# Kernel optimization log

Measured on AMD Instinct MI355X. Metric: run time of the kernel, lower is better.

The kernel has to match this reference:

```python
import jax, jax.numpy as jnp
import numpy as np
import math

H, C = 16, 4


def _clustering(x, alv, mu, log_var, log_prior, mi_estimation):
    # x: [B,h,L,D], alv: [B,h,L], mu/log_var: [h or 1, C, D], log_prior: [h or 1, C]
    B, Hh, L, D = x.shape
    z = x  # eval mode: no reparameterization noise
    zd = z[:, :, :, None, :]                       # [B,h,L,1,D]
    mu_b = mu[:, None, :, :]                       # [h,1,C,D]
    lv = log_var[:, None, :, :]
    var = jnp.exp(lv)
    lp = jax.nn.log_softmax(log_prior, axis=-1)    # [h,C]
    mse = (zd - mu_b) ** 2 / var                   # [B,h,L,C,D]
    log_pdf = -0.5 * mse.sum(-1) - 0.5 * lv.sum(-1) - D * math.pi  # [B,h,L,C]
    log_pdf = log_pdf + lp[:, None, :]
    shift = jax.lax.stop_gradient(log_pdf.max(axis=-1, keepdims=True))
    log_probs = jax.nn.log_softmax(log_pdf - shift + 5.0, axis=-1)
    cp = jnp.exp(log_probs)                        # cluster probs [B,h,L,C]
    lp_b = jnp.broadcast_to(lp[None, :, None, :], log_probs.shape)
    # F.kl_div(log_probs, prior) = prior * (log prior - log_probs)
    kl = (jnp.exp(lp_b) * (lp_b - log_probs)).sum(-1).mean(axis=(1, 2))
    alv5 = alv[:, :, :, None, None]
    avar = jnp.exp(alv5)
    kl = kl + 0.5 * (cp * (mse + avar / var + lv).sum(-1)).sum(-1).mean(axis=(1, 2))
    kl = kl - 0.5 * ((1.0 + alv5).sum(-1) * D).mean(axis=(1, 2, 3))
    eye = jnp.eye(L, dtype=x.dtype)
    div = jnp.einsum('bhqc,bhkc->bhqk', cp, cp)
    div = ((div - eye) ** 2) * (eye * 1.25 + (1.0 - eye) * 0.75)
    div_loss = div.mean(axis=(1, 2, 3))
    if mi_estimation:
        pdf = jnp.exp(log_pdf - jax.lax.stop_gradient(log_pdf.max())).sum(-1, keepdims=True)
        w = cp * pdf
        mi_probs = w / jnp.maximum(w.sum(axis=2, keepdims=True), 1e-6)  # L1 normalize over L
        mi_p = jnp.minimum(jnp.einsum('bilc,bjlc->blij', mi_probs, cp), 1.0)
        mask_h = 1.0 - jnp.eye(Hh, dtype=x.dtype)
        mi_loss = -(jnp.log(1.0 - mi_p + 1e-6) * mask_h).mean(axis=(1, 2, 3)) * 10.0
        aff = jnp.einsum('bhqc,bhkc->bhqk', cp, cp)
        diag = jnp.diagonal(jax.nn.log_softmax(aff, axis=-1), axis1=2, axis2=3)
        mi_loss = mi_loss - diag.mean(axis=(1, 2))
    else:
        mi_loss = jnp.zeros_like(kl)
    return z, cp, kl, div_loss, mi_loss


def _forward(query, key, value, Wq, bq, Wk, bk, Wv, bv, Wo, bo, Wsem, bsem,
             Whead, bhead, tok_mu, tok_log_var, tok_log_prior,
             head_mu, head_log_var, head_log_prior):
    B, L, D = query.shape
    Dk = D // H
    q = query @ Wq + bq
    k = key @ Wk + bk
    v = value @ Wv + bv
    alv = (q @ Wsem + bsem).transpose(0, 2, 1)                 # [B,H,L]
    qh = q.reshape(B, L, H, Dk).transpose(0, 2, 1, 3)          # [B,H,L,Dk]
    z, cp_q, kl_q, div_q, _ = _clustering(qh, alv, tok_mu, tok_log_var, tok_log_prior, False)
    kh = k.reshape(B, L, H, Dk).transpose(0, 2, 1, 3)
    vh = v.reshape(B, L, H, Dk).transpose(0, 2, 1, 3)
    cluster_mask = jnp.einsum('bhqc,bhkc->bhqk', cp_q, cp_q)   # token-cluster affinity mask
    scores = jnp.einsum('bhqd,bhkd->bhqk', z, kh) / math.sqrt(Dk)
    attn = jax.nn.softmax(scores, axis=-1) * cluster_mask
    attn = attn / (attn.sum(axis=-1, keepdims=True) + 1e-6)
    ctx = jnp.einsum('bhqk,bhkd->bhqd', attn, vh)              # [B,H,L,Dk]
    ctx_f = ctx.transpose(0, 2, 1, 3).reshape(B, L, D)
    alv_h = (ctx_f @ Whead + bhead).transpose(0, 2, 1)         # [B,H,L]
    _, cp_h, kl_h, div_h, mi = _clustering(ctx, alv_h, head_mu, head_log_var, head_log_prior, True)
    out = ctx_f @ Wo + bo
    return out, attn.mean(axis=1), kl_q + kl_h, div_q + div_h, mi


def setup_inputs() -> dict:
    key = jax.random.key(0)
    ks = jax.random.split(key, 12)
    B, L, D = 8, 512, 1024
    Dk = D // H
    s = 1.0 / math.sqrt(D)
    f32 = jnp.float32
    inp = {
        'query': jax.random.normal(ks[0], (B, L, D), f32),
        'key': jax.random.normal(ks[1], (B, L, D), f32),
        'value': jax.random.normal(ks[2], (B, L, D), f32),
        'Wq': jax.random.normal(ks[3], (D, D), f32) * s, 'bq': jnp.zeros((D,), f32),
        'Wk': jax.random.normal(ks[4], (D, D), f32) * s, 'bk': jnp.zeros((D,), f32),
        'Wv': jax.random.normal(ks[5], (D, D), f32) * s, 'bv': jnp.zeros((D,), f32),
        'Wo': jax.random.normal(ks[6], (D, D), f32) * s, 'bo': jnp.zeros((D,), f32),
        'Wsem': jax.random.normal(ks[7], (D, H), f32) * s, 'bsem': jnp.zeros((H,), f32),
        'Whead': jax.random.normal(ks[8], (D, H), f32) * s, 'bhead': jnp.zeros((H,), f32),
        'tok_mu': jax.random.normal(ks[9], (H, C, Dk), f32) * 0.1,
        'tok_log_var': jnp.zeros((H, C, Dk), f32),
        'tok_log_prior': jnp.full((H, C), math.log(1.0 / C), f32),
        'head_mu': jax.random.normal(ks[10], (1, C, Dk), f32) * 0.1,
        'head_log_var': jnp.zeros((1, C, Dk), f32),
        'head_log_prior': jnp.full((1, C), math.log(1.0 / C), f32),
    }
    return inp


def reference(query, key, value, Wq, bq, Wk, bk, Wv, bv, Wo, bo, Wsem, bsem,
              Whead, bhead, tok_mu, tok_log_var, tok_log_prior,
              head_mu, head_log_var, head_log_prior):
    return _forward(query, key, value, Wq, bq, Wk, bk, Wv, bv, Wo, bo, Wsem, bsem,
                    Whead, bhead, tok_mu, tok_log_var, tok_log_prior,
                    head_mu, head_log_var, head_log_prior)
```

## Files before the change

kernel.cpp:

```cpp
#include <hip/hip_runtime.h>
#include <math.h>

#define BB 8
#define LL 512
#define DD 1024
#define HH 16
#define CC 4
#define DK 64
#define NEG_DPI 201.06192982974676f

typedef __attribute__((ext_vector_type(8))) short short8;
typedef __attribute__((ext_vector_type(4))) float floatx4;
typedef __attribute__((ext_vector_type(8))) unsigned short u16x8;
typedef __attribute__((ext_vector_type(4))) unsigned short u16x4;

__device__ inline float block_sum256(float v, float* s_red) {
    int t = threadIdx.x;
    s_red[t] = v; __syncthreads();
    for (int off = 128; off > 0; off >>= 1) {
        if (t < off) s_red[t] += s_red[t + off];
        __syncthreads();
    }
    float r = s_red[0]; __syncthreads();
    return r;
}
__device__ inline float block_max256(float v, float* s_red) {
    int t = threadIdx.x;
    s_red[t] = v; __syncthreads();
    for (int off = 128; off > 0; off >>= 1) {
        if (t < off) s_red[t] = fmaxf(s_red[t], s_red[t + off]);
        __syncthreads();
    }
    float r = s_red[0]; __syncthreads();
    return r;
}
__device__ inline unsigned int fenc(float f) {
    unsigned int b = __float_as_uint(f);
    return (b & 0x80000000u) ? ~b : (b | 0x80000000u);
}
__device__ inline float fdec(unsigned int u) {
    return (u & 0x80000000u) ? __uint_as_float(u ^ 0x80000000u) : __uint_as_float(~u);
}
__device__ inline unsigned short f2bf(float x) {
    unsigned int u = __float_as_uint(x);
    return (unsigned short)((u + 0x7FFFu + ((u >> 16) & 1u)) >> 16);
}
__device__ inline float bf2f(unsigned short h) {
    return __uint_as_float((unsigned int)h << 16);
}

__global__ __launch_bounds__(256)
void convert_hilo(const float* __restrict__ x, unsigned short* __restrict__ hh,
                  unsigned short* __restrict__ ll) {
    int i = blockIdx.x * 256 + threadIdx.x;
    float4 v = ((const float4*)x)[i];
    u16x4 h, l;
    float c[4] = {v.x, v.y, v.z, v.w};
#pragma unroll
    for (int j = 0; j < 4; j++) {
        unsigned short hb = f2bf(c[j]);
        h[j] = hb;
        l[j] = f2bf(c[j] - bf2f(hb));
    }
    ((u16x4*)hh)[i] = h;
    ((u16x4*)ll)[i] = l;
}

__global__ __launch_bounds__(256)
void wconv4(const float* __restrict__ W0, const float* __restrict__ W1,
            const float* __restrict__ W2, const float* __restrict__ W3,
            unsigned short* __restrict__ Tbase) {
    __shared__ float tile[64][65];
    int z = blockIdx.z;
    const float* W = (z == 0) ? W0 : (z == 1) ? W1 : (z == 2) ? W2 : W3;
    const size_t WS = (size_t)DD * DD;
    unsigned short* Th = Tbase + (size_t)z * 2 * WS;
    unsigned short* Tl = Th + WS;
    int t = threadIdx.x;
    int n0 = blockIdx.x * 64, k0 = blockIdx.y * 64;
    int r = t >> 4, c4 = (t & 15) * 4;
#pragma unroll
    for (int rr = 0; rr < 64; rr += 16) {
        float4 v = *(const float4*)&W[(size_t)(k0 + r + rr) * DD + n0 + c4];
        tile[r + rr][c4 + 0] = v.x; tile[r + rr][c4 + 1] = v.y;
        tile[r + rr][c4 + 2] = v.z; tile[r + rr][c4 + 3] = v.w;
    }
    __syncthreads();
    int rn = t >> 2, kg = (t & 3) * 16;
    u16x8 oh[2], ol[2];
#pragma unroll
    for (int j = 0; j < 16; j++) {
        float x = tile[kg + j][rn];
        unsigned short hb = f2bf(x);
        oh[j >> 3][j & 7] = hb;
        ol[j >> 3][j & 7] = f2bf(x - bf2f(hb));
    }
    size_t o = (size_t)(n0 + rn) * DD + k0 + kg;
    *(u16x8*)&Th[o] = oh[0]; *(u16x8*)&Th[o + 8] = oh[1];
    *(u16x8*)&Tl[o] = ol[0]; *(u16x8*)&Tl[o + 8] = ol[1];
}

__device__ __forceinline__
void gemm_body(const unsigned short* __restrict__ Ah, const unsigned short* __restrict__ Al,
               const unsigned short* __restrict__ Bh, const unsigned short* __restrict__ Bl,
               const float* __restrict__ bias, float* __restrict__ C,
               unsigned short* __restrict__ Ch, unsigned short* __restrict__ Cl) {
    __shared__ unsigned short sAh[128 * 32];
    __shared__ unsigned short sAl[128 * 32];
    __shared__ unsigned short sBh[128 * 32];
    __shared__ unsigned short sBl[128 * 32];
    int t = threadIdx.x;
    int n0 = blockIdx.x * 128, m0 = blockIdx.y * 128;
    int lane = t & 63, w = t >> 6;
    int wm = w >> 1, wn = w & 1;
    int lm = lane & 15, quad = lane >> 4;
    int srow = t >> 1, sk = (t & 1) * 16;

    const unsigned short* gAh = Ah + (size_t)(m0 + srow) * DD + sk;
    const unsigned short* gAl = Al + (size_t)(m0 + srow) * DD + sk;
    const unsigned short* gBh = Bh + (size_t)(n0 + srow) * DD + sk;
    const unsigned short* gBl = Bl + (size_t)(n0 + srow) * DD + sk;
    unsigned short* wAh = &sAh[srow * 32 + sk];
    unsigned short* wAl = &sAl[srow * 32 + sk];
    unsigned short* wBh = &sBh[srow * 32 + sk];
    unsigned short* wBl = &sBl[srow * 32 + sk];

    floatx4 acc[4][4] = {};

    for (int kt = 0; kt < 32; kt++) {
        int kb = kt * 32;
        u16x8 a0 = *(const u16x8*)(gAh + kb);
        u16x8 a1 = *(const u16x8*)(gAh + kb + 8);
        u16x8 a2 = *(const u16x8*)(gAl + kb);
        u16x8 a3 = *(const u16x8*)(gAl + kb + 8);
        u16x8 b0 = *(const u16x8*)(gBh + kb);
        u16x8 b1 = *(const u16x8*)(gBh + kb + 8);
        u16x8 b2 = *(const u16x8*)(gBl + kb);
        u16x8 b3 = *(const u16x8*)(gBl + kb + 8);
        __syncthreads();
        *(u16x8*)(wAh) = a0; *(u16x8*)(wAh + 8) = a1;
        *(u16x8*)(wAl) = a2; *(u16x8*)(wAl + 8) = a3;
        *(u16x8*)(wBh) = b0; *(u16x8*)(wBh + 8) = b1;
        *(u16x8*)(wBl) = b2; *(u16x8*)(wBl + 8) = b3;
        __syncthreads();

        short8 bh[4], bl[4];
#pragma unroll
        for (int j = 0; j < 4; j++) {
            int nb = (wn * 64 + j * 16 + lm) * 32 + quad * 8;
            bh[j] = *(const short8*)&sBh[nb];
            bl[j] = *(const short8*)&sBl[nb];
        }
#pragma unroll
        for (int i = 0; i < 4; i++) {
            int ab = (wm * 64 + i * 16 + lm) * 32 + quad * 8;
            short8 ah = *(const short8*)&sAh[ab];
            short8 al = *(const short8*)&sAl[ab];
#pragma unroll
            for (int j = 0; j < 4; j++) {
                acc[i][j] = __builtin_amdgcn_mfma_f32_16x16x32_bf16(ah, bh[j], acc[i][j], 0, 0, 0);
                acc[i][j] = __builtin_amdgcn_mfma_f32_16x16x32_bf16(ah, bl[j], acc[i][j], 0, 0, 0);
                acc[i][j] = __builtin_amdgcn_mfma_f32_16x16x32_bf16(al, bh[j], acc[i][j], 0, 0, 0);
            }
        }
    }
#pragma unroll
    for (int i = 0; i < 4; i++) {
#pragma unroll
        for (int j = 0; j < 4; j++) {
            int n = n0 + wn * 64 + j * 16 + lm;
            float bv = bias[n];
#pragma unroll
            for (int r = 0; r < 4; r++) {
                int m = m0 + wm * 64 + i * 16 + quad * 4 + r;
                size_t idx = (size_t)m * DD + n;
                float val = acc[i][j][r] + bv;
                if (C) C[idx] = val;
                if (Ch) {
                    unsigned short hb = f2bf(val);
                    Ch[idx] = hb;
                    Cl[idx] = f2bf(val - bf2f(hb));
                }
            }
        }
    }
}

__global__ __launch_bounds__(256)
void mfma_gemm_bias(const unsigned short* __restrict__ Ah, const unsigned short* __restrict__ Al,
                    const unsigned short* __restrict__ Bh, const unsigned short* __restrict__ Bl,
                    const float* __restrict__ bias, float* __restrict__ C,
                    unsigned short* __restrict__ Ch, unsigned short* __restrict__ Cl) {
    gemm_body(Ah, Al, Bh, Bl, bias, C, Ch, Cl);
}

__global__ __launch_bounds__(256)
void mfma_gemm_qkv(const unsigned short* __restrict__ ist3, const unsigned short* __restrict__ wbase,
                   const float* __restrict__ bq, const float* __restrict__ bk,
                   const float* __restrict__ bv, float* __restrict__ Cq,
                   unsigned short* __restrict__ obase) {
    int z = blockIdx.z;
    const size_t NB = (size_t)BB * LL * DD;
    const size_t WS = (size_t)DD * DD;
    const unsigned short* Ah = ist3 + (size_t)z * 2 * NB;
    const unsigned short* Bh = wbase + (size_t)z * 2 * WS;
    const float* bias = (z == 0) ? bq : (z == 1) ? bk : bv;
    float* C = (z == 0) ? Cq : nullptr;
    unsigned short* Ch = obase + (size_t)z * 2 * NB;
    gemm_body(Ah, Ah + NB, Bh, Bh + WS, bias, C, Ch, Ch + NB);
}

__global__ __launch_bounds__(256)
void vt_prep2(const unsigned short* __restrict__ voh, const unsigned short* __restrict__ vol,
              unsigned short* __restrict__ vth, unsigned short* __restrict__ vtl) {
    __shared__ unsigned short tile[128 * 68];
    int t = threadIdx.x;
    int which = blockIdx.x & 1;
    int l0 = (blockIdx.x >> 1) * 128, h = blockIdx.y, b = blockIdx.z;
    const unsigned short* src = which ? vol : voh;
    unsigned short* dst = which ? vtl : vth;
#pragma unroll
    for (int i = 0; i < 8; i++) {
        int u = t + i * 256;
        int l = u >> 4, c4 = (u & 15) * 4;
        u16x4 v4 = *(const u16x4*)&src[((size_t)(b * LL + l0 + l)) * DD + h * DK + c4];
        tile[l * 68 + c4 + 0] = v4[0]; tile[l * 68 + c4 + 1] = v4[1];
        tile[l * 68 + c4 + 2] = v4[2]; tile[l * 68 + c4 + 3] = v4[3];
    }
    __syncthreads();
    size_t ob = ((size_t)(b * HH + h)) * DK * LL;
#pragma unroll
    for (int i = 0; i < 8; i++) {
        int u = t + i * 256;
        int d = u >> 5, lq = (u & 31) * 4;
        u16x4 o;
#pragma unroll
        for (int j = 0; j < 4; j++) o[j] = tile[(lq + j) * 68 + d];
        *(u16x4*)&dst[ob + (size_t)d * LL + l0 + lq] = o;
    }
}

__global__ __launch_bounds__(256)
void alv_gemm(const float* __restrict__ A, const float* __restrict__ Wp,
              const float* __restrict__ bias, float* __restrict__ alv) {
    __shared__ float As[16][65];
    __shared__ float Ws[64][17];
    int t = threadIdx.x;
    int m0 = blockIdx.x * 16;
    int r = t >> 4, hh = t & 15;
    float acc = 0.f;
    for (int kt = 0; kt < 16; kt++) {
        __syncthreads();
#pragma unroll
        for (int i = 0; i < 4; i++) {
            int e = t + i * 256;
            int rr = e >> 6, kk = e & 63;
            As[rr][kk] = A[(size_t)(m0 + rr) * DD + kt * 64 + kk];
        }
#pragma unroll
        for (int i = 0; i < 4; i++) {
            int e = t + i * 256;
            int kk = e >> 4, h2 = e & 15;
            Ws[kk][h2] = Wp[(size_t)(kt * 64 + kk) * HH + h2];
        }
        __syncthreads();
#pragma unroll
        for (int kk = 0; kk < 64; kk++) acc += As[r][kk] * Ws[kk][hh];
    }
    int m = m0 + r;
    int b = m >> 9, l = m & 511;
    alv[(size_t)(b * HH + hh) * LL + l] = acc + bias[hh];
}

__global__ __launch_bounds__(256)
void cluster_kernel(const float* __restrict__ zsrc, const float* __restrict__ alv,
                    const float* __restrict__ mu, const float* __restrict__ logvar,
                    const float* __restrict__ logprior,
                    float* __restrict__ cp_out, float* __restrict__ lpdf_out,
                    unsigned int* __restrict__ maxenc, float* __restrict__ kl_out,
                    int isHead) {
    __shared__ float s_mu[CC * DK], s_iv[CC * DK], s_lv[CC * DK];
    __shared__ float s_slv[CC], s_siv[CC], s_lp[CC];
    __shared__ float s_red[256];
    int t = threadIdx.x;
    int tile = blockIdx.x & 1;
    int bh = blockIdx.x >> 1;
    int h = bh & (HH - 1), b = bh >> 4;
    int hm = isHead ? 0 : h;

    {
        float m = mu[hm * CC * DK + t];
        float lv = logvar[hm * CC * DK + t];
        s_mu[t] = m; s_lv[t] = lv; s_iv[t] = expf(-lv);
    }
    __syncthreads();
    if (t < CC) {
        float slv = 0.f, siv = 0.f;
        for (int d = 0; d < DK; d++) { slv += s_lv[t * DK + d]; siv += s_iv[t * DK + d]; }
        s_slv[t] = slv; s_siv[t] = siv;
    }
    if (t == CC) {
        float x[CC];
        float m = -1e30f;
        for (int c = 0; c < CC; c++) { x[c] = logprior[hm * CC + c]; m = fmaxf(m, x[c]); }
        float se = 0.f;
        for (int c = 0; c < CC; c++) se += expf(x[c] - m);
        float lse = m + logf(se);
        for (int c = 0; c < CC; c++) s_lp[c] = x[c] - lse;
    }
    __syncthreads();

    int l = tile * 256 + t;
    const float* zp = zsrc + ((size_t)(b * LL + l)) * DD + h * DK;
    float acc[CC] = {0.f, 0.f, 0.f, 0.f};
    for (int d = 0; d < DK; d += 4) {
        float4 z4 = *(const float4*)(zp + d);
#pragma unroll
        for (int c = 0; c < CC; c++) {
            float d0 = z4.x - s_mu[c * DK + d];     acc[c] += d0 * d0 * s_iv[c * DK + d];
            float d1 = z4.y - s_mu[c * DK + d + 1]; acc[c] += d1 * d1 * s_iv[c * DK + d + 1];
            float d2 = z4.z - s_mu[c * DK + d + 2]; acc[c] += d2 * d2 * s_iv[c * DK + d + 2];
            float d3 = z4.w - s_mu[c * DK + d + 3]; acc[c] += d3 * d3 * s_iv[c * DK + d + 3];
        }
    }
    float lpdf[CC];
#pragma unroll
    for (int c = 0; c < CC; c++)
        lpdf[c] = -0.5f * acc[c] - 0.5f * s_slv[c] - NEG_DPI + s_lp[c];
    float m = fmaxf(fmaxf(lpdf[0], lpdf[1]), fmaxf(lpdf[2], lpdf[3]));
    float se = 0.f;
#pragma unroll
    for (int c = 0; c < CC; c++) se += expf(lpdf[c] - m);
    float lse = m + logf(se);
    float lprob[CC], cpv[CC];
    size_t idx = ((size_t)(bh * LL + l)) * CC;
#pragma unroll
    for (int c = 0; c < CC; c++) {
        lprob[c] = lpdf[c] - lse;
        cpv[c] = expf(lprob[c]);
        cp_out[idx + c] = cpv[c];
    }
    if (isHead) {
#pragma unroll
        for (int c = 0; c < CC; c++) lpdf_out[idx + c] = lpdf[c];
    }
    float alvv = alv[(size_t)bh * LL + l];
    float avar = expf(alvv);
    float t1 = 0.f, t2 = 0.f;
#pragma unroll
    for (int c = 0; c < CC; c++) {
        t1 += expf(s_lp[c]) * (s_lp[c] - lprob[c]);
        t2 += cpv[c] * (acc[c] + avar * s_siv[c] + s_slv[c]);
    }
    float klv = t1 + 0.5f * t2 - 0.5f * (float)DK * (1.0f + alvv);
    float tot = block_sum256(klv, s_red);
    if (t == 0) atomicAdd(kl_out + b, tot * (1.0f / (HH * LL)));
    if (isHead) {
        float mt = block_max256(m, s_red);
        if (t == 0) atomicMax(maxenc, fenc(mt));
    }
}

__global__ __launch_bounds__(256)
void pairstats_kernel(const float* __restrict__ cp, float* __restrict__ div_out,
                      float* __restrict__ mi_out, int isHead) {
    __shared__ float s_cp[LL * CC];
    __shared__ float s_red[256];
    int t = threadIdx.x;
    int bh = blockIdx.x >> 3;
    int seg = blockIdx.x & 7;
    int b = bh >> 4;
    const float* base = cp + (size_t)bh * LL * CC;
#pragma unroll
    for (int i = 0; i < 2; i++) {
        int e = t + i * 256;
        *(float4*)&s_cp[e * 4] = *(const float4*)&base[e * 4];
    }
    __syncthreads();

    int q = seg * 64 + (t >> 2);
    int ln = t & 3;
    float4 cq = *(float4*)&s_cp[q * 4];
    float divacc = 0.f, m = -1e30f, s = 0.f, selfdot = 0.f;
    for (int k = ln; k < LL; k += 4) {
        float4 ck = *(float4*)&s_cp[k * 4];
        float dot = cq.x * ck.x + cq.y * ck.y + cq.z * ck.z + cq.w * ck.w;
        float del = (k == q) ? 1.f : 0.f;
        float dd = dot - del;
        divacc += dd * dd * (0.75f + 0.5f * del);
        if (isHead) {
            if (dot > m) { s = s * expf(m - dot) + 1.f; m = dot; }
            else         { s += expf(dot - m); }
            if (k == q) selfdot = dot;
        }
    }
#pragma unroll
    for (int off = 1; off <= 2; off <<= 1) divacc += __shfl_xor(divacc, off, 64);
    float diag = 0.f;
    if (isHead) {
#pragma unroll
        for (int off = 1; off <= 2; off <<= 1) {
            float om = __shfl_xor(m, off, 64);
            float os = __shfl_xor(s, off, 64);
            float nm = fmaxf(m, om);
            s = s * expf(m - nm) + os * expf(om - nm);
            m = nm;
        }
#pragma unroll
        for (int off = 1; off <= 2; off <<= 1) selfdot += __shfl_xor(selfdot, off, 64);
        diag = selfdot - (m + logf(s));
    }
    float dtot = block_sum256(ln == 0 ? divacc : 0.f, s_red);
    if (t == 0) atomicAdd(div_out + b, dtot * (1.0f / ((float)HH * LL * LL)));
    if (isHead) {
        float gtot = block_sum256(ln == 0 ? diag : 0.f, s_red);
        if (t == 0) atomicAdd(mi_out + b, -gtot * (1.0f / (HH * LL)));
    }
}

__global__ __launch_bounds__(256)
void attn3_kernel(const unsigned short* __restrict__ qoh, const unsigned short* __restrict__ qol,
                  const unsigned short* __restrict__ koh, const unsigned short* __restrict__ kol,
                  const unsigned short* __restrict__ vth, const unsigned short* __restrict__ vtl,
                  const float* __restrict__ cpq,
                  float* __restrict__ ctxf, unsigned short* __restrict__ cxh,
                  unsigned short* __restrict__ cxl,
                  float* __restrict__ attn_h, int h0) {
    __shared__ __align__(16) char sbuf[33280];
    __shared__ float s_inv[16];
    float* S = (float*)sbuf;
    unsigned short* Ph = (unsigned short*)sbuf;
    unsigned short* Pl = Ph + 16 * 520;

    int t = threadIdx.x;
    int id = blockIdx.x;
    int xcd = id & 7;
    int sid = id >> 3;
    int qt = sid & 31;
    int combo = ((sid >> 5) << 3) | xcd;
    int hl = combo & 7;
    int b = combo >> 3;
    int h = h0 + hl;
    int q0 = qt * 16;
    int lane = t & 63, w = t >> 6;
    int lm = lane & 15, quad = lane >> 4;
    int bh = b * HH + h;

    size_t qbase = ((size_t)(b * LL + q0 + lm)) * DD + h * DK + quad * 8;
    short8 qah0 = *(const short8*)(qoh + qbase);
    short8 qah1 = *(const short8*)(qoh + qbase + 32);
    short8 qal0 = *(const short8*)(qol + qbase);
    short8 qal1 = *(const short8*)(qol + qbase + 32);

    floatx4 sa[8] = {};
#pragma unroll
    for (int j = 0; j < 8; j++) {
        int n0 = w * 128 + j * 16;
        size_t kbase = ((size_t)(b * LL + n0 + lm)) * DD + h * DK + quad * 8;
        short8 kbh0 = *(const short8*)(koh + kbase);
        short8 kbh1 = *(const short8*)(koh + kbase + 32);
        short8 kbl0 = *(const short8*)(kol + kbase);
        short8 kbl1 = *(const short8*)(kol + kbase + 32);
        sa[j] = __builtin_amdgcn_mfma_f32_16x16x32_bf16(qah0, kbh0, sa[j], 0, 0, 0);
        sa[j] = __builtin_amdgcn_mfma_f32_16x16x32_bf16(qah1, kbh1, sa[j], 0, 0, 0);
        sa[j] = __builtin_amdgcn_mfma_f32_16x16x32_bf16(qah0, kbl0, sa[j], 0, 0, 0);
        sa[j] = __builtin_amdgcn_mfma_f32_16x16x32_bf16(qah1, kbl1, sa[j], 0, 0, 0);
        sa[j] = __builtin_amdgcn_mfma_f32_16x16x32_bf16(qal0, kbh0, sa[j], 0, 0, 0);
        sa[j] = __builtin_amdgcn_mfma_f32_16x16x32_bf16(qal1, kbh1, sa[j], 0, 0, 0);
    }
#pragma unroll
    for (int j = 0; j < 8; j++) {
        int kc = w * 128 + j * 16 + lm;
#pragma unroll
        for (int r = 0; r < 4; r++)
            S[(quad * 4 + r) * 516 + kc] = sa[j][r] * 0.125f;
    }
    __syncthreads();

    {
        int r = t >> 4, ln = t & 15;
        const float4* cpb = (const float4*)(cpq + (size_t)bh * LL * CC);
        float m = -1e30f;
        for (int k = ln; k < LL; k += 16) m = fmaxf(m, S[r * 516 + k]);
#pragma unroll
        for (int off = 8; off > 0; off >>= 1) m = fmaxf(m, __shfl_xor(m, off, 16));
        float4 cq = cpb[q0 + r];
        float Z = 0.f, Sm = 0.f;
        for (int k = ln; k < LL; k += 16) {
            float e = expf(S[r * 516 + k] - m);
            float4 ck = cpb[k];
            float mask = cq.x * ck.x + cq.y * ck.y + cq.z * ck.z + cq.w * ck.w;
            float a = e * mask;
            Z += e; Sm += a;
            S[r * 516 + k] = a;
        }
#pragma unroll
        for (int off = 8; off > 0; off >>= 1) {
            Z += __shfl_xor(Z, off, 16);
            Sm += __shfl_xor(Sm, off, 16);
        }
        if (ln == 0) s_inv[r] = 1.f / (Sm + 1e-6f * Z);
    }
    __syncthreads();

    float4 pv[8];
#pragma unroll
    for (int i = 0; i < 8; i++) {
        int e = t + i * 256;
        int r2 = e >> 7, k4 = (e & 127) * 4;
        float4 p = *(float4*)&S[r2 * 516 + k4];
        float inv = s_inv[r2];
        p.x *= inv; p.y *= inv; p.z *= inv; p.w *= inv;
        pv[i] = p;
        *(float4*)&attn_h[(((size_t)((b * 8 + hl) * LL + q0 + r2)) * LL) + k4] = p;
    }
    __syncthreads();
#pragma unroll
    for (int i = 0; i < 8; i++) {
        int e = t + i * 256;
        int r2 = e >> 7, k4 = (e & 127) * 4;
        float c[4] = {pv[i].x, pv[i].y, pv[i].z, pv[i].w};
        u16x4 hv, lv;
#pragma unroll
        for (int j = 0; j < 4; j++) {
            unsigned short hb = f2bf(c[j]);
            hv[j] = hb;
            lv[j] = f2bf(c[j] - bf2f(hb));
        }
        *(u16x4*)&Ph[r2 * 520 + k4] = hv;
        *(u16x4*)&Pl[r2 * 520 + k4] = lv;
    }
    __syncthreads();

    int dn = w * 16 + lm;
    const unsigned short* vrh = vth + ((size_t)bh * DK + dn) * LL;
    const unsigned short* vrl = vtl + ((size_t)bh * DK + dn) * LL;
    floatx4 ca = {};
#pragma unroll
    for (int kc = 0; kc < 16; kc++) {
        int kb = kc * 32 + quad * 8;
        short8 pah = *(const short8*)&Ph[lm * 520 + kb];
        short8 pal = *(const short8*)&Pl[lm * 520 + kb];
        short8 vbh = *(const short8*)(vrh + kb);
        short8 vbl = *(const short8*)(vrl + kb);
        ca = __builtin_amdgcn_mfma_f32_16x16x32_bf16(pah, vbh, ca, 0, 0, 0);
        ca = __builtin_amdgcn_mfma_f32_16x16x32_bf16(pah, vbl, ca, 0, 0, 0);
        ca = __builtin_amdgcn_mfma_f32_16x16x32_bf16(pal, vbh, ca, 0, 0, 0);
    }
#pragma unroll
    for (int r = 0; r < 4; r++) {
        float val = ca[r];
        size_t idx = ((size_t)(b * LL + q0 + quad * 4 + r)) * DD + h * DK + dn;
        ctxf[idx] = val;
        unsigned short hb = f2bf(val);
        cxh[idx] = hb;
        cxl[idx] = f2bf(val - bf2f(hb));
    }
}

__global__ __launch_bounds__(256)
void attn_reduce(const float* __restrict__ attn_h, float* __restrict__ attn_out,
                 int accumulate) {
    int e = blockIdx.x * 256 + threadIdx.x;
    int b = e >> 16;
    int rem = e & 65535;
    float4 s = {0.f, 0.f, 0.f, 0.f};
#pragma unroll
    for (int hl = 0; hl < 8; hl++) {
        float4 v = ((const float4*)attn_h)[(((size_t)(b * 8 + hl)) << 16) + rem];
        s.x += v.x; s.y += v.y; s.z += v.z; s.w += v.w;
    }
    float4* o = (float4*)attn_out + (((size_t)b) << 16) + rem;
    const float sc = 1.0f / (float)HH;
    float4 prev = {0.f, 0.f, 0.f, 0.f};
    if (accumulate) prev = *o;
    prev.x += s.x * sc; prev.y += s.y * sc; prev.z += s.z * sc; prev.w += s.w * sc;
    *o = prev;
}

__global__ __launch_bounds__(256)
void wsum_kernel(const float* __restrict__ lpdf, const float* __restrict__ cp,
                 const unsigned int* __restrict__ maxenc,
                 float* __restrict__ pdf_out, float* __restrict__ wsum_out) {
    __shared__ float s_red[256];
    int t = threadIdx.x;
    int bh = blockIdx.x;
    float M = fdec(*maxenc);
    float a[CC] = {0.f, 0.f, 0.f, 0.f};
    for (int li = 0; li < 2; li++) {
        int l = t + li * 256;
        size_t idx = ((size_t)bh * LL + l) * CC;
        float p0 = expf(lpdf[idx + 0] - M);
        float p1 = expf(lpdf[idx + 1] - M);
        float p2 = expf(lpdf[idx + 2] - M);
        float p3 = expf(lpdf[idx + 3] - M);
        float pd = p0 + p1 + p2 + p3;
        pdf_out[(size_t)bh * LL + l] = pd;
        a[0] += cp[idx + 0] * pd; a[1] += cp[idx + 1] * pd;
        a[2] += cp[idx + 2] * pd; a[3] += cp[idx + 3] * pd;
    }
#pragma unroll
    for (int c = 0; c < CC; c++) {
        float tot = block_sum256(a[c], s_red);
        if (t == 0) wsum_out[bh * CC + c] = tot;
    }
}

__global__ __launch_bounds__(256)
void mi_kernel(const float* __restrict__ cp, const float* __restrict__ pdf,
               const float* __restrict__ wsum, float* __restrict__ mi_out) {
    __shared__ float s_q[HH * CC];
    __shared__ float s_c[HH * CC];
    __shared__ float s_red[256];
    int t = threadIdx.x;
    int b = blockIdx.x >> 9;
    int l = blockIdx.x & 511;
    if (t < HH * CC) {
        int i = t >> 2, c = t & 3;
        float cpv = cp[((size_t)(b * HH + i) * LL + l) * CC + c];
        s_c[t] = cpv;
        float w = cpv * pdf[(size_t)(b * HH + i) * LL + l];
        float ws = wsum[(b * HH + i) * CC + c];
        s_q[t] = w / fmaxf(ws, 1e-6f);
    }
    __syncthreads();
    int i = t >> 4, j = t & 15;
    float sdot = 0.f;
#pragma unroll
    for (int c = 0; c < CC; c++) sdot += s_q[i * 4 + c] * s_c[j * 4 + c];
    float mi_p = fminf(sdot, 1.f);
    float val = (i != j) ? logf(1.f - mi_p + 1e-6f) : 0.f;
    float tot = block_sum256(val, s_red);
    if (t == 0) atomicAdd(mi_out + b, -10.f * tot * (1.0f / ((float)LL * HH * HH)));
}

extern "C" void kernel_launch(void* const* d_in, const int* in_sizes, int n_in,
                              void* d_out, int out_size, void* d_ws, size_t ws_size,
                              hipStream_t stream) {
    (void)in_sizes; (void)n_in; (void)out_size; (void)ws_size;
    const float* query  = (const float*)d_in[0];
    const float* key    = (const float*)d_in[1];
    const float* value  = (const float*)d_in[2];
    const float* Wq     = (const float*)d_in[3];
    const float* bq     = (const float*)d_in[4];
    const float* Wk     = (const float*)d_in[5];
    const float* bk     = (const float*)d_in[6];
    const float* Wv     = (const float*)d_in[7];
    const float* bv     = (const float*)d_in[8];
    const float* Wo     = (const float*)d_in[9];
    const float* bo     = (const float*)d_in[10];
    const float* Wsem   = (const float*)d_in[11];
    const float* bsem   = (const float*)d_in[12];
    const float* Whead  = (const float*)d_in[13];
    const float* bhead  = (const float*)d_in[14];
    const float* tokmu  = (const float*)d_in[15];
    const float* toklv  = (const float*)d_in[16];
    const float* toklp  = (const float*)d_in[17];
    const float* headmu = (const float*)d_in[18];
    const float* headlv = (const float*)d_in[19];
    const float* headlp = (const float*)d_in[20];

    float* ws   = (float*)d_ws;
    const size_t NBLD = (size_t)BB * LL * DD;
    float* q    = ws;
    float* ctxf = ws + NBLD;
    float* alvq = ws + 2 * NBLD;
    float* alvh = alvq + (size_t)BB * HH * LL;
    float* cpq  = alvh + (size_t)BB * HH * LL;
    float* cph  = cpq + (size_t)BB * HH * LL * CC;
    float* lpdfh= cph + (size_t)BB * HH * LL * CC;
    float* pdfb = lpdfh + (size_t)BB * HH * LL * CC;
    float* wsumb= pdfb + (size_t)BB * HH * LL;
    unsigned int* maxenc = (unsigned int*)(wsumb + (size_t)BB * HH * CC);
    float* scr3 = (float*)(maxenc + 4);

    unsigned short* us = (unsigned short*)(scr3 + (size_t)BB * 8 * LL * LL);
    const size_t WSZ = (size_t)DD * DD;
    unsigned short* ist_h = us;
    unsigned short* ist_l = ist_h + NBLD;
    unsigned short* qoh = ist_l + NBLD;
    unsigned short* qol = qoh + NBLD;
    unsigned short* koh = qol + NBLD;
    unsigned short* kol = koh + NBLD;
    unsigned short* voh = kol + NBLD;
    unsigned short* vol = voh + NBLD;
    unsigned short* vth = vol + NBLD;
    unsigned short* vtl = vth + NBLD;
    unsigned short* wqh = vtl + NBLD;
    unsigned short* wql = wqh + WSZ;
    unsigned short* wkh = wql + WSZ;
    unsigned short* wkl = wkh + WSZ;
    unsigned short* wvh = wkl + WSZ;
    unsigned short* wvl = wvh + WSZ;
    unsigned short* woh = wvl + WSZ;
    unsigned short* wol = woh + WSZ;

    unsigned short* ist3 = (unsigned short*)scr3;
    float* attn_h = scr3;

    float* out      = (float*)d_out;
    float* attn_out = out + NBLD;
    float* kl_out   = attn_out + (size_t)BB * LL * LL;
    float* div_out  = kl_out + BB;
    float* mi_out   = div_out + BB;

    hipMemsetAsync(kl_out, 0, 3 * BB * sizeof(float), stream);
    hipMemsetAsync(maxenc, 0, sizeof(unsigned int), stream);

    wconv4<<<dim3(16, 16, 4), 256, 0, stream>>>(Wq, Wk, Wv, Wo, wqh);

    convert_hilo<<<NBLD / 1024, 256, 0, stream>>>(query, ist3,            ist3 + NBLD);
    convert_hilo<<<NBLD / 1024, 256, 0, stream>>>(key,   ist3 + 2 * NBLD, ist3 + 3 * NBLD);
    convert_hilo<<<NBLD / 1024, 256, 0, stream>>>(value, ist3 + 4 * NBLD, ist3 + 5 * NBLD);
    mfma_gemm_qkv<<<dim3(DD / 128, BB * LL / 128, 3), 256, 0, stream>>>(
        ist3, wqh, bq, bk, bv, q, qoh);

    vt_prep2<<<dim3(2 * LL / 128, HH, BB), 256, 0, stream>>>(voh, vol, vth, vtl);

    alv_gemm<<<BB * LL / 16, 256, 0, stream>>>(q, Wsem, bsem, alvq);
    cluster_kernel<<<BB * HH * 2, 256, 0, stream>>>(q, alvq, tokmu, toklv, toklp,
                                                    cpq, nullptr, nullptr, kl_out, 0);
    pairstats_kernel<<<BB * HH * 8, 256, 0, stream>>>(cpq, div_out, nullptr, 0);

    for (int h0 = 0; h0 < HH; h0 += 8) {
        attn3_kernel<<<dim3(2048), 256, 0, stream>>>(
            qoh, qol, koh, kol, vth, vtl, cpq, ctxf, ist_h, ist_l, attn_h, h0);
        attn_reduce<<<BB * LL * LL / 4 / 256, 256, 0, stream>>>(
            attn_h, attn_out, h0 > 0 ? 1 : 0);
    }

    alv_gemm<<<BB * LL / 16, 256, 0, stream>>>(ctxf, Whead, bhead, alvh);
    cluster_kernel<<<BB * HH * 2, 256, 0, stream>>>(ctxf, alvh, headmu, headlv, headlp,
                                                    cph, lpdfh, maxenc, kl_out, 1);
    pairstats_kernel<<<BB * HH * 8, 256, 0, stream>>>(cph, div_out, mi_out, 1);
    wsum_kernel<<<BB * HH, 256, 0, stream>>>(lpdfh, cph, maxenc, pdfb, wsumb);
    mi_kernel<<<BB * LL, 256, 0, stream>>>(cph, pdfb, wsumb, mi_out);
    mfma_gemm_bias<<<dim3(DD / 128, BB * LL / 128), 256, 0, stream>>>(
        ist_h, ist_l, woh, wol, bo, out, nullptr, nullptr);
}
```

Measured before the change: 795.7 us.

## Swizzle GEMM LDS layout, prefetch next k-tile, remap blocks per XCD

The shared bf16 hi/lo GEMM now XOR-swizzles its LDS tile layout to avoid bank conflicts on the MFMA fragment reads. It also register-prefetches the next k-tile's global loads while the current tile computes. The QKV and output GEMMs switch to a 1D grid whose block ids are remapped so each XCD gets contiguous row bands, aiming for better L2 reuse of A and B tiles. This adds register pressure from the prefetch buffers and hardcodes the grid sizes into the index math.

After: 764.0 us. -4.0%, faster.

```diff
diff --git a/kernel.cpp b/kernel.cpp
--- a/kernel.cpp
+++ b/kernel.cpp
@@ -104,13 +104,13 @@
 void gemm_body(const unsigned short* __restrict__ Ah, const unsigned short* __restrict__ Al,
                const unsigned short* __restrict__ Bh, const unsigned short* __restrict__ Bl,
                const float* __restrict__ bias, float* __restrict__ C,
-               unsigned short* __restrict__ Ch, unsigned short* __restrict__ Cl) {
+               unsigned short* __restrict__ Ch, unsigned short* __restrict__ Cl,
+               int m0, int n0) {
     __shared__ unsigned short sAh[128 * 32];
     __shared__ unsigned short sAl[128 * 32];
     __shared__ unsigned short sBh[128 * 32];
     __shared__ unsigned short sBl[128 * 32];
     int t = threadIdx.x;
-    int n0 = blockIdx.x * 128, m0 = blockIdx.y * 128;
     int lane = t & 63, w = t >> 6;
     int wm = w >> 1, wn = w & 1;
     int lm = lane & 15, quad = lane >> 4;
@@ -120,47 +120,52 @@
     const unsigned short* gAl = Al + (size_t)(m0 + srow) * DD + sk;
     const unsigned short* gBh = Bh + (size_t)(n0 + srow) * DD + sk;
     const unsigned short* gBl = Bl + (size_t)(n0 + srow) * DD + sk;
-    unsigned short* wAh = &sAh[srow * 32 + sk];
-    unsigned short* wAl = &sAl[srow * 32 + sk];
-    unsigned short* wBh = &sBh[srow * 32 + sk];
-    unsigned short* wBl = &sBl[srow * 32 + sk];
+    int f = (srow >> 1) & 3;
+    int s0 = (t & 1) * 2;
+    int ws0 = srow * 32 + ((s0 ^ f) * 8);
+    int ws1 = srow * 32 + (((s0 | 1) ^ f) * 8);
 
     floatx4 acc[4][4] = {};
+    u16x8 a0, a1, a2, a3, b0, b1, b2, b3;
+    a0 = *(const u16x8*)(gAh);     a1 = *(const u16x8*)(gAh + 8);
+    a2 = *(const u16x8*)(gAl);     a3 = *(const u16x8*)(gAl + 8);
+    b0 = *(const u16x8*)(gBh);     b1 = *(const u16x8*)(gBh + 8);
+    b2 = *(const u16x8*)(gBl);     b3 = *(const u16x8*)(gBl + 8);
 
     for (int kt = 0; kt < 32; kt++) {
-        int kb = kt * 32;
-        u16x8 a0 = *(const u16x8*)(gAh + kb);
-        u16x8 a1 = *(const u16x8*)(gAh + kb + 8);
-        u16x8 a2 = *(const u16x8*)(gAl + kb);
-        u16x8 a3 = *(const u16x8*)(gAl + kb + 8);
-        u16x8 b0 = *(const u16x8*)(gBh + kb);
-        u16x8 b1 = *(const u16x8*)(gBh + kb + 8);
-        u16x8 b2 = *(const u16x8*)(gBl + kb);
-        u16x8 b3 = *(const u16x8*)(gBl + kb + 8);
         __syncthreads();
-        *(u16x8*)(wAh) = a0; *(u16x8*)(wAh + 8) = a1;
-        *(u16x8*)(wAl) = a2; *(u16x8*)(wAl + 8) = a3;
-        *(u16x8*)(wBh) = b0; *(u16x8*)(wBh + 8) = b1;
-        *(u16x8*)(wBl) = b2; *(u16x8*)(wBl + 8) = b3;
+        *(u16x8*)&sAh[ws0] = a0; *(u16x8*)&sAh[ws1] = a1;
+        *(u16x8*)&sAl[ws0] = a2; *(u16x8*)&sAl[ws1] = a3;
+        *(u16x8*)&sBh[ws0] = b0; *(u16x8*)&sBh[ws1] = b1;
+        *(u16x8*)&sBl[ws0] = b2; *(u16x8*)&sBl[ws1] = b3;
         __syncthreads();
-
-        short8 bh[4], bl[4];
+        if (kt < 31) {
+            int kb = (kt + 1) * 32;
+            a0 = *(const u16x8*)(gAh + kb); a1 = *(const u16x8*)(gAh + kb + 8);
+            a2 = *(const u16x8*)(gAl + kb); a3 = *(const u16x8*)(gAl + kb + 8);
+            b0 = *(const u16x8*)(gBh + kb); b1 = *(const u16x8*)(gBh + kb + 8);
+            b2 = *(const u16x8*)(gBl + kb); b3 = *(const u16x8*)(gBl + kb + 8);
+        }
+
+        short8 bhf[4], blf[4];
 #pragma unroll
         for (int j = 0; j < 4; j++) {
-            int nb = (wn * 64 + j * 16 + lm) * 32 + quad * 8;
-            bh[j] = *(const short8*)&sBh[nb];
-            bl[j] = *(const short8*)&sBl[nb];
+            int nrow = wn * 64 + j * 16 + lm;
+            int nb = nrow * 32 + ((quad ^ ((nrow >> 1) & 3)) * 8);
+            bhf[j] = *(const short8*)&sBh[nb];
+            blf[j] = *(const short8*)&sBl[nb];
         }
 #pragma unroll
         for (int i = 0; i < 4; i++) {
-            int ab = (wm * 64 + i * 16 + lm) * 32 + quad * 8;
+            int arow = wm * 64 + i * 16 + lm;
+            int ab = arow * 32 + ((quad ^ ((arow >> 1) & 3)) * 8);
             short8 ah = *(const short8*)&sAh[ab];
             short8 al = *(const short8*)&sAl[ab];
 #pragma unroll
             for (int j = 0; j < 4; j++) {
-                acc[i][j] = __builtin_amdgcn_mfma_f32_16x16x32_bf16(ah, bh[j], acc[i][j], 0, 0, 0);
-                acc[i][j] = __builtin_amdgcn_mfma_f32_16x16x32_bf16(ah, bl[j], acc[i][j], 0, 0, 0);
-                acc[i][j] = __builtin_amdgcn_mfma_f32_16x16x32_bf16(al, bh[j], acc[i][j], 0, 0, 0);
+                acc[i][j] = __builtin_amdgcn_mfma_f32_16x16x32_bf16(ah, bhf[j], acc[i][j], 0, 0, 0);
+                acc[i][j] = __builtin_amdgcn_mfma_f32_16x16x32_bf16(ah, blf[j], acc[i][j], 0, 0, 0);
+                acc[i][j] = __builtin_amdgcn_mfma_f32_16x16x32_bf16(al, bhf[j], acc[i][j], 0, 0, 0);
             }
         }
     }
@@ -191,7 +196,11 @@
                     const unsigned short* __restrict__ Bh, const unsigned short* __restrict__ Bl,
                     const float* __restrict__ bias, float* __restrict__ C,
                     unsigned short* __restrict__ Ch, unsigned short* __restrict__ Cl) {
-    gemm_body(Ah, Al, Bh, Bl, bias, C, Ch, Cl);
+    int id = blockIdx.x;
+    int xcd = id & 7, s = id >> 3;
+    int y = xcd * 4 + (s >> 3);
+    int x = s & 7;
+    gemm_body(Ah, Al, Bh, Bl, bias, C, Ch, Cl, y * 128, x * 128);
 }
 
 __global__ __launch_bounds__(256)
@@ -199,7 +208,12 @@
                    const float* __restrict__ bq, const float* __restrict__ bk,
                    const float* __restrict__ bv, float* __restrict__ Cq,
                    unsigned short* __restrict__ obase) {
-    int z = blockIdx.z;
+    int id = blockIdx.x;
+    int xcd = id & 7, s = id >> 3;
+    int p = xcd * 12 + (s >> 3);
+    int x = s & 7;
+    int z = p >> 5;
+    int y = p & 31;
     const size_t NB = (size_t)BB * LL * DD;
     const size_t WS = (size_t)DD * DD;
     const unsigned short* Ah = ist3 + (size_t)z * 2 * NB;
@@ -207,7 +221,7 @@
     const float* bias = (z == 0) ? bq : (z == 1) ? bk : bv;
     float* C = (z == 0) ? Cq : nullptr;
     unsigned short* Ch = obase + (size_t)z * 2 * NB;
-    gemm_body(Ah, Ah + NB, Bh, Bh + WS, bias, C, Ch, Ch + NB);
+    gemm_body(Ah, Ah + NB, Bh, Bh + WS, bias, C, Ch, Ch + NB, y * 128, x * 128);
 }
 
 __global__ __launch_bounds__(256)
@@ -712,7 +726,7 @@
     convert_hilo<<<NBLD / 1024, 256, 0, stream>>>(query, ist3,            ist3 + NBLD);
     convert_hilo<<<NBLD / 1024, 256, 0, stream>>>(key,   ist3 + 2 * NBLD, ist3 + 3 * NBLD);
     convert_hilo<<<NBLD / 1024, 256, 0, stream>>>(value, ist3 + 4 * NBLD, ist3 + 5 * NBLD);
-    mfma_gemm_qkv<<<dim3(DD / 128, BB * LL / 128, 3), 256, 0, stream>>>(
+    mfma_gemm_qkv<<<dim3(768), 256, 0, stream>>>(
         ist3, wqh, bq, bk, bv, q, qoh);
 
     vt_prep2<<<dim3(2 * LL / 128, HH, BB), 256, 0, stream>>>(voh, vol, vth, vtl);
@@ -735,6 +749,6 @@
     pairstats_kernel<<<BB * HH * 8, 256, 0, stream>>>(cph, div_out, mi_out, 1);
     wsum_kernel<<<BB * HH, 256, 0, stream>>>(lpdfh, cph, maxenc, pdfb, wsumb);
     mi_kernel<<<BB * LL, 256, 0, stream>>>(cph, pdfb, wsumb, mi_out);
-    mfma_gemm_bias<<<dim3(DD / 128, BB * LL / 128), 256, 0, stream>>>(
+    mfma_gemm_bias<<<dim3(256), 256, 0, stream>>>(
         ist_h, ist_l, woh, wol, bo, out, nullptr, nullptr);
 }
```
